# Optimization experiments

Measured on AMD Instinct MI355X. Metric: run time of the kernel, lower is better.

Reference implementation:

```python
import jax, jax.numpy as jnp
import numpy as np

VOCAB = 50257
EMBED = 512
HEADS = 16
DHEAD = 64
HIDDEN = HEADS * DHEAD
BATCH = 4096
SEQ = 16  # 2 * window_size


def setup_inputs() -> dict:
    key = jax.random.key(0)
    ks = jax.random.split(key, 9)
    inp = {
        "t": jax.random.randint(ks[0], (BATCH,), 0, VOCAB, dtype=jnp.int64 if jax.config.jax_enable_x64 else jnp.int32),
        "c": jax.random.randint(ks[1], (BATCH, SEQ), 0, VOCAB, dtype=jnp.int64 if jax.config.jax_enable_x64 else jnp.int32),
        "emb": jax.random.normal(ks[2], (VOCAB, EMBED), dtype=jnp.float32),
        "WQ": jax.random.normal(ks[3], (HIDDEN, EMBED), dtype=jnp.float32) * (EMBED ** -0.5),
        "bQ": jnp.zeros((HIDDEN,), dtype=jnp.float32),
        "WK": jax.random.normal(ks[4], (HIDDEN, EMBED), dtype=jnp.float32) * (EMBED ** -0.5),
        "bK": jnp.zeros((HIDDEN,), dtype=jnp.float32),
        "WV": jax.random.normal(ks[5], (HIDDEN, EMBED), dtype=jnp.float32) * (EMBED ** -0.5),
        "bV": jnp.zeros((HIDDEN,), dtype=jnp.float32),
    }
    return inp


def reference(t, c, emb, WQ, bQ, WK, bK, WV, bV):
    B = t.shape[0]
    S = c.shape[1]
    target = emb[t]            # [B, E]
    context = emb[c]           # [B, S, E]
    # batched projections (replaces the per-element Python loops)
    Q = (target @ WQ.T + bQ).reshape(B, HEADS, DHEAD)          # [B, H, Dh]
    K = (context @ WK.T + bK).reshape(B, S, HEADS, DHEAD)      # [B, S, H, Dh]
    V = (context @ WV.T + bV).reshape(B, S, HEADS, DHEAD)      # [B, S, H, Dh]
    # W[b,s,h,g] = sum_d Q[b,h,d] * K[b,s,g,d] / sqrt(Dh)  (head-x-head scores, faithful to source)
    scores = jnp.einsum('bhd,bsgd->bshg', Q, K) * (DHEAD ** -0.5)
    A = jax.nn.softmax(scores, axis=-1)                         # softmax over key-head axis
    tmp = jnp.einsum('bshg,bsgd->bshd', A, V).reshape(B, S, HIDDEN)
    context_vector = jnp.sum(tmp, axis=1)                       # [B, HIDDEN]
    target_vector = target @ WV.T + bV                          # [B, HIDDEN]
    return (target_vector, context_vector)
```

## Files before the change

kernel.cpp:

```cpp
#include <hip/hip_runtime.h>
#include <stdint.h>

#define VOCAB 50257
#define EMBED 512
#define HIDDEN 1024
#define BATCH 4096
#define SEQ 16

typedef __attribute__((ext_vector_type(8))) short short8;
typedef __attribute__((ext_vector_type(4))) float f32x4;
typedef __attribute__((ext_vector_type(4))) int int4v;
typedef __attribute__((ext_vector_type(4))) float float4v;

__device__ __forceinline__ uint32_t f2bfu(float f) {
  uint32_t u = __builtin_bit_cast(uint32_t, f);
  return (u + 0x7FFFu + ((u >> 16) & 1u)) >> 16;
}

__device__ __forceinline__ int4v pack8(float4v a, float4v b) {
  int4v r;
  r.x = (int)(f2bfu(a.x) | (f2bfu(a.y) << 16));
  r.y = (int)(f2bfu(a.z) | (f2bfu(a.w) << 16));
  r.z = (int)(f2bfu(b.x) | (f2bfu(b.y) << 16));
  r.w = (int)(f2bfu(b.z) | (f2bfu(b.w) << 16));
  return r;
}

__device__ __forceinline__ void gload16(const void* g, void* l) {
  __builtin_amdgcn_global_load_lds((const __attribute__((address_space(1))) void*)g,
                                   (__attribute__((address_space(3))) void*)l,
                                   16, 0, 0);
}

__global__ void prep_emb_k(const float* __restrict__ emb, ushort* __restrict__ dst, int n8) {
  int i = blockIdx.x * 256 + threadIdx.x;
  if (i >= n8) return;
  size_t e = (size_t)i * 8;
  float4v a = *(const float4v*)(emb + e);
  float4v b = *(const float4v*)(emb + e + 4);
  *(int4v*)(dst + e) = pack8(a, b);
}

__global__ void prep_w_k(const float* __restrict__ WQ, const float* __restrict__ WK,
                         const float* __restrict__ WV, ushort* __restrict__ Wkv,
                         ushort* __restrict__ Wqv) {
  int i = blockIdx.x * 256 + threadIdx.x;
  int which = i >> 17;
  int j = i & 0x1FFFF;
  size_t e = (size_t)j * 8;
  int row = (int)(e >> 9);
  int col = (int)(e & 511);
  const float* src = (which == 0)
      ? ((row < 1024) ? WK + (size_t)row * 512 + col : WV + (size_t)(row - 1024) * 512 + col)
      : ((row < 1024) ? WQ + (size_t)row * 512 + col : WV + (size_t)(row - 1024) * 512 + col);
  float4v a = *(const float4v*)(src);
  float4v b = *(const float4v*)(src + 4);
  ushort* dst = (which == 0) ? Wkv : Wqv;
  *(int4v*)(dst + e) = pack8(a, b);
}

template <int EPI>
__global__ __launch_bounds__(256) void gemm_k(
    const ushort* __restrict__ Aemb, const int* __restrict__ tok,
    const ushort* __restrict__ W, const float* __restrict__ bias_lo,
    const float* __restrict__ bias_hi, ushort* __restrict__ out_lo,
    void* __restrict__ out_hi_) {
  __shared__ ushort At[128 * 32];
  __shared__ ushort Bt[128 * 32];
  const int t = threadIdx.x;
  const int wave = t >> 6, lane = t & 63;
  const int mb = blockIdx.x, nb = blockIdx.y;
  const int r0 = t >> 2;
  const int acol = (t & 3) * 8;
  const int tok0 = tok[mb * 128 + r0];
  const int tok1 = tok[mb * 128 + 64 + r0];
  const ushort* asrc0 = Aemb + (size_t)tok0 * EMBED + acol;
  const ushort* asrc1 = Aemb + (size_t)tok1 * EMBED + acol;
  const ushort* bsrc0 = W + (size_t)(nb * 128 + r0) * EMBED + acol;
  const ushort* bsrc1 = W + (size_t)(nb * 128 + 64 + r0) * EMBED + acol;
  char* aD0 = (char*)At + wave * 1024;
  char* aD1 = (char*)At + 4096 + wave * 1024;
  char* bD0 = (char*)Bt + wave * 1024;
  char* bD1 = (char*)Bt + 4096 + wave * 1024;
  const int wm = wave >> 1, wn = wave & 1;
  const int fr = lane & 15, fu = lane >> 4;
  f32x4 acc[4][4] = {};
  for (int kt = 0; kt < 16; ++kt) {
    const int k0 = kt * 32;
    gload16(asrc0 + k0, aD0);
    gload16(asrc1 + k0, aD1);
    gload16(bsrc0 + k0, bD0);
    gload16(bsrc1 + k0, bD1);
    __syncthreads();
    short8 af[4], bf[4];
#pragma unroll
    for (int mi = 0; mi < 4; ++mi)
      af[mi] = *(const short8*)(At + (wm * 64 + mi * 16 + fr) * 32 + fu * 8);
#pragma unroll
    for (int ni = 0; ni < 4; ++ni)
      bf[ni] = *(const short8*)(Bt + (wn * 64 + ni * 16 + fr) * 32 + fu * 8);
#pragma unroll
    for (int mi = 0; mi < 4; ++mi)
#pragma unroll
      for (int ni = 0; ni < 4; ++ni)
        acc[mi][ni] = __builtin_amdgcn_mfma_f32_16x16x32_bf16(af[mi], bf[ni], acc[mi][ni], 0, 0, 0);
    __syncthreads();
  }
#pragma unroll
  for (int ni = 0; ni < 4; ++ni) {
    const int nloc = nb * 128 + wn * 64 + ni * 16 + fr;
    if (nb < 8) {
      const float bv = bias_lo[nloc];
#pragma unroll
      for (int mi = 0; mi < 4; ++mi)
#pragma unroll
        for (int r = 0; r < 4; ++r) {
          const int m = mb * 128 + wm * 64 + mi * 16 + fu * 4 + r;
          out_lo[(size_t)m * 1024 + nloc] = (ushort)f2bfu(acc[mi][ni][r] + bv);
        }
    } else {
      const int n = nloc - 1024;
      const float bv = bias_hi[n];
      if (EPI == 0) {
        ushort* Vb = (ushort*)out_hi_;
        const int g = n >> 6, d = n & 63;
        const int offv = (d >> 4) * 256 + (g >> 3) * 128 + (d & 15) * 8 + (g & 7);
#pragma unroll
        for (int mi = 0; mi < 4; ++mi)
#pragma unroll
          for (int r = 0; r < 4; ++r) {
            const int m = mb * 128 + wm * 64 + mi * 16 + fu * 4 + r;
            Vb[(size_t)m * 1024 + offv] = (ushort)f2bfu(acc[mi][ni][r] + bv);
          }
      } else {
        float* o0 = (float*)out_hi_;
#pragma unroll
        for (int mi = 0; mi < 4; ++mi)
#pragma unroll
          for (int r = 0; r < 4; ++r) {
            const int m = mb * 128 + wm * 64 + mi * 16 + fu * 4 + r;
            o0[(size_t)m * 1024 + n] = acc[mi][ni][r] + bv;
          }
      }
    }
  }
}

__global__ __launch_bounds__(256) void attn_k(const ushort* __restrict__ Qb,
                                              const ushort* __restrict__ Kb,
                                              const ushort* __restrict__ Vb,
                                              float* __restrict__ out1) {
  const int wave = threadIdx.x >> 6, lane = threadIdx.x & 63;
  const int b = blockIdx.x * 4 + wave;
  const int u = lane >> 4, col = lane & 15;
  const ushort* qrow = Qb + (size_t)b * 1024;
  const short8 qf0 = *(const short8*)(qrow + col * 64 + u * 8);
  const short8 qf1 = *(const short8*)(qrow + col * 64 + u * 8 + 32);
  f32x4 accd[4] = {};
  const int srcA = (col + ((u & 1) << 5)) << 2;
  for (int s = 0; s < 16; ++s) {
    const size_t m = (size_t)b * 16 + s;
    const ushort* krow = Kb + m * 1024;
    const short8 kf0 = *(const short8*)(krow + col * 64 + u * 8);
    const short8 kf1 = *(const short8*)(krow + col * 64 + u * 8 + 32);
    f32x4 sc = {};
    sc = __builtin_amdgcn_mfma_f32_16x16x32_bf16(kf0, qf0, sc, 0, 0, 0);
    sc = __builtin_amdgcn_mfma_f32_16x16x32_bf16(kf1, qf1, sc, 0, 0, 0);
    float x0 = sc[0] * 0.125f, x1 = sc[1] * 0.125f;
    float x2 = sc[2] * 0.125f, x3 = sc[3] * 0.125f;
    float mx = fmaxf(fmaxf(x0, x1), fmaxf(x2, x3));
    mx = fmaxf(mx, __shfl_xor(mx, 16));
    mx = fmaxf(mx, __shfl_xor(mx, 32));
    float p0 = __expf(x0 - mx), p1 = __expf(x1 - mx);
    float p2 = __expf(x2 - mx), p3 = __expf(x3 - mx);
    float sm = p0 + p1 + p2 + p3;
    sm += __shfl_xor(sm, 16);
    sm += __shfl_xor(sm, 32);
    const float inv = 1.0f / sm;
    const uint32_t w01 = f2bfu(p0 * inv) | (f2bfu(p1 * inv) << 16);
    const uint32_t w23 = f2bfu(p2 * inv) | (f2bfu(p3 * inv) << 16);
    int d0 = __builtin_amdgcn_ds_bpermute(srcA, (int)w01);
    int d1 = __builtin_amdgcn_ds_bpermute(srcA, (int)w23);
    int d2 = __builtin_amdgcn_ds_bpermute(srcA + 64, (int)w01);
    int d3 = __builtin_amdgcn_ds_bpermute(srcA + 64, (int)w23);
    if (lane >= 32) { d0 = 0; d1 = 0; d2 = 0; d3 = 0; }
    int4v ww;
    ww.x = d0; ww.y = d1; ww.z = d2; ww.w = d3;
    const short8 af = __builtin_bit_cast(short8, ww);
    const ushort* vrow = Vb + m * 1024;
#pragma unroll
    for (int dblk = 0; dblk < 4; ++dblk) {
      const short8 vf = *(const short8*)(vrow + dblk * 256 + (u & 1) * 128 + col * 8);
      accd[dblk] = __builtin_amdgcn_mfma_f32_16x16x32_bf16(af, vf, accd[dblk], 0, 0, 0);
    }
  }
  float* orow = out1 + (size_t)b * 1024;
#pragma unroll
  for (int dblk = 0; dblk < 4; ++dblk)
#pragma unroll
    for (int r = 0; r < 4; ++r)
      orow[(u * 4 + r) * 64 + dblk * 16 + col] = accd[dblk][r];
}

extern "C" void kernel_launch(void* const* d_in, const int* in_sizes, int n_in,
                              void* d_out, int out_size, void* d_ws, size_t ws_size,
                              hipStream_t stream) {
  (void)in_sizes; (void)n_in; (void)out_size; (void)ws_size;
  const int* t = (const int*)d_in[0];
  const int* c = (const int*)d_in[1];
  const float* emb = (const float*)d_in[2];
  const float* WQ = (const float*)d_in[3];
  const float* bQ = (const float*)d_in[4];
  const float* WK = (const float*)d_in[5];
  const float* bK = (const float*)d_in[6];
  const float* WV = (const float*)d_in[7];
  const float* bV = (const float*)d_in[8];
  float* out0 = (float*)d_out;
  float* out1 = out0 + (size_t)BATCH * HIDDEN;

  char* ws = (char*)d_ws;
  size_t off = 0;
  ushort* embb = (ushort*)(ws + off);
  off += ((size_t)VOCAB * EMBED * 2 + 255) & ~(size_t)255;
  ushort* Wkv = (ushort*)(ws + off); off += (size_t)2048 * 512 * 2;
  ushort* Wqv = (ushort*)(ws + off); off += (size_t)2048 * 512 * 2;
  ushort* Qb = (ushort*)(ws + off); off += (size_t)BATCH * HIDDEN * 2;
  ushort* Kb = (ushort*)(ws + off); off += (size_t)BATCH * SEQ * HIDDEN * 2;
  ushort* Vb = (ushort*)(ws + off); off += (size_t)BATCH * SEQ * HIDDEN * 2;

  const int n8 = VOCAB * EMBED / 8;
  prep_emb_k<<<(n8 + 255) / 256, 256, 0, stream>>>(emb, embb, n8);
  prep_w_k<<<1024, 256, 0, stream>>>(WQ, WK, WV, Wkv, Wqv);
  dim3 gc(BATCH * SEQ / 128, 16);
  gemm_k<0><<<gc, 256, 0, stream>>>(embb, c, Wkv, bK, bV, Kb, (void*)Vb);
  dim3 gt(BATCH / 128, 16);
  gemm_k<1><<<gt, 256, 0, stream>>>(embb, t, Wqv, bQ, bV, Qb, (void*)out0);
  attn_k<<<BATCH / 4, 256, 0, stream>>>(Qb, Kb, Vb, out1);
}
```

Baseline: 598.0 us.

## Double-buffer GEMM LDS tiles and swap grid axes for row-block reuse

```diff
diff --git a/kernel.cpp b/kernel.cpp
--- a/kernel.cpp
+++ b/kernel.cpp
@@ -65,11 +65,11 @@
     const ushort* __restrict__ W, const float* __restrict__ bias_lo,
     const float* __restrict__ bias_hi, ushort* __restrict__ out_lo,
     void* __restrict__ out_hi_) {
-  __shared__ ushort At[128 * 32];
-  __shared__ ushort Bt[128 * 32];
+  __shared__ ushort At[2 * 128 * 32];
+  __shared__ ushort Bt[2 * 128 * 32];
   const int t = threadIdx.x;
   const int wave = t >> 6, lane = t & 63;
-  const int mb = blockIdx.x, nb = blockIdx.y;
+  const int nb = blockIdx.x, mb = blockIdx.y;
   const int r0 = t >> 2;
   const int acol = (t & 3) * 8;
   const int tok0 = tok[mb * 128 + r0];
@@ -78,33 +78,41 @@
   const ushort* asrc1 = Aemb + (size_t)tok1 * EMBED + acol;
   const ushort* bsrc0 = W + (size_t)(nb * 128 + r0) * EMBED + acol;
   const ushort* bsrc1 = W + (size_t)(nb * 128 + 64 + r0) * EMBED + acol;
-  char* aD0 = (char*)At + wave * 1024;
-  char* aD1 = (char*)At + 4096 + wave * 1024;
-  char* bD0 = (char*)Bt + wave * 1024;
-  char* bD1 = (char*)Bt + 4096 + wave * 1024;
   const int wm = wave >> 1, wn = wave & 1;
   const int fr = lane & 15, fu = lane >> 4;
+
+  auto stage = [&](int buf, int kt) {
+    const int k0 = kt * 32;
+    char* ab = (char*)At + buf * 8192 + wave * 1024;
+    char* bb = (char*)Bt + buf * 8192 + wave * 1024;
+    gload16(asrc0 + k0, ab);
+    gload16(asrc1 + k0, ab + 4096);
+    gload16(bsrc0 + k0, bb);
+    gload16(bsrc1 + k0, bb + 4096);
+  };
+
   f32x4 acc[4][4] = {};
+  stage(0, 0);
+  __syncthreads();
+  int cur = 0;
   for (int kt = 0; kt < 16; ++kt) {
-    const int k0 = kt * 32;
-    gload16(asrc0 + k0, aD0);
-    gload16(asrc1 + k0, aD1);
-    gload16(bsrc0 + k0, bD0);
-    gload16(bsrc1 + k0, bD1);
-    __syncthreads();
+    if (kt < 15) stage(cur ^ 1, kt + 1);
+    const ushort* Ab = At + cur * 4096;
+    const ushort* Bb = Bt + cur * 4096;
     short8 af[4], bf[4];
 #pragma unroll
     for (int mi = 0; mi < 4; ++mi)
-      af[mi] = *(const short8*)(At + (wm * 64 + mi * 16 + fr) * 32 + fu * 8);
+      af[mi] = *(const short8*)(Ab + (wm * 64 + mi * 16 + fr) * 32 + fu * 8);
 #pragma unroll
     for (int ni = 0; ni < 4; ++ni)
-      bf[ni] = *(const short8*)(Bt + (wn * 64 + ni * 16 + fr) * 32 + fu * 8);
+      bf[ni] = *(const short8*)(Bb + (wn * 64 + ni * 16 + fr) * 32 + fu * 8);
 #pragma unroll
     for (int mi = 0; mi < 4; ++mi)
 #pragma unroll
       for (int ni = 0; ni < 4; ++ni)
         acc[mi][ni] = __builtin_amdgcn_mfma_f32_16x16x32_bf16(af[mi], bf[ni], acc[mi][ni], 0, 0, 0);
     __syncthreads();
+    cur ^= 1;
   }
 #pragma unroll
   for (int ni = 0; ni < 4; ++ni) {
@@ -231,9 +239,9 @@
   const int n8 = VOCAB * EMBED / 8;
   prep_emb_k<<<(n8 + 255) / 256, 256, 0, stream>>>(emb, embb, n8);
   prep_w_k<<<1024, 256, 0, stream>>>(WQ, WK, WV, Wkv, Wqv);
-  dim3 gc(BATCH * SEQ / 128, 16);
+  dim3 gc(16, BATCH * SEQ / 128);
   gemm_k<0><<<gc, 256, 0, stream>>>(embb, c, Wkv, bK, bV, Kb, (void*)Vb);
-  dim3 gt(BATCH / 128, 16);
+  dim3 gt(16, BATCH / 128);
   gemm_k<1><<<gt, 256, 0, stream>>>(embb, t, Wqv, bQ, bV, Qb, (void*)out0);
   attn_k<<<BATCH / 4, 256, 0, stream>>>(Qb, Kb, Vb, out1);
 }
```

After: 587.3 us. No clear change (-1.8%).
